# Optimization experiments

Measured on AMD Instinct MI355X. Metric: run time of the kernel, lower is better.

Reference implementation:

```python
import jax, jax.numpy as jnp
import numpy as np

NUM_CLASS = 3
SCORE_THRESH = 0.1
NMS_THRESH = 0.25
PRE = 512    # NMS_PRE_MAXSIZE (reduced from 4096 for memory; same algorithm)
POST = 100   # NMS_POST_MAXSIZE
EPS = 1e-8


def _cross(a, b):
    return a[..., 0] * b[..., 1] - a[..., 1] * b[..., 0]


def _corners(box):
    # box: (7,) = (x, y, z, dx, dy, dz, heading) -> BEV corners (4,2), CCW
    x, y, dx, dy, r = box[0], box[1], box[3], box[4], box[6]
    c, s = jnp.cos(r), jnp.sin(r)
    lx = jnp.array([0.5, -0.5, -0.5, 0.5]) * dx
    ly = jnp.array([0.5, 0.5, -0.5, -0.5]) * dy
    return jnp.stack([x + lx * c - ly * s, y + lx * s + ly * c], axis=-1)


def _in_box(pts, box):
    # pts (P,2): point-in-rotated-rect test in the box frame
    px, py = pts[:, 0] - box[0], pts[:, 1] - box[1]
    c, s = jnp.cos(box[6]), jnp.sin(box[6])
    u = px * c + py * s
    v = -px * s + py * c
    return (jnp.abs(u) <= box[3] * 0.5 + 1e-5) & (jnp.abs(v) <= box[4] * 0.5 + 1e-5)


def _bev_inter_area(ba, bb):
    # Exact rotated-rect intersection area (same construction as the CUDA
    # iou3d kernel: inside corners + edge intersections, angle-sorted shoelace).
    ca, cb = _corners(ba), _corners(bb)
    pa, ra = ca, jnp.roll(ca, -1, 0) - ca       # edges of a
    pb, rb = cb, jnp.roll(cb, -1, 0) - cb       # edges of b
    d = _cross(ra[:, None, :], rb[None, :, :])  # (4,4)
    dsafe = jnp.where(jnp.abs(d) > EPS, d, 1.0)
    qp = pb[None, :, :] - pa[:, None, :]
    t = _cross(qp, rb[None, :, :]) / dsafe
    u = _cross(qp, ra[:, None, :]) / dsafe
    vi = (jnp.abs(d) > EPS) & (t >= 0.0) & (t <= 1.0) & (u >= 0.0) & (u <= 1.0)
    ip = pa[:, None, :] + t[..., None] * ra[:, None, :]  # (4,4,2)
    pts = jnp.concatenate([ca, cb, ip.reshape(16, 2)], 0)          # (24,2)
    val = jnp.concatenate([_in_box(ca, bb), _in_box(cb, ba), vi.reshape(16)], 0)
    cnt = val.sum()
    ctr = (pts * val[:, None]).sum(0) / jnp.maximum(cnt, 1)
    ang = jnp.where(val, jnp.arctan2(pts[:, 1] - ctr[1], pts[:, 0] - ctr[0]), 1e9)
    o = jnp.argsort(ang)
    ps, vs = pts[o], val[o]
    ps = jnp.where(vs[:, None], ps, ps[0])  # collapse invalid onto first valid pt
    area = 0.5 * jnp.abs(_cross(ps, jnp.roll(ps, -1, 0)).sum())
    return jnp.where(cnt >= 3, area, 0.0)


def _iou3d(ba, bb):
    inter = _bev_inter_area(ba, bb)
    zt = jnp.minimum(ba[2] + ba[5] * 0.5, bb[2] + bb[5] * 0.5)
    zb = jnp.maximum(ba[2] - ba[5] * 0.5, bb[2] - bb[5] * 0.5)
    i3 = inter * jnp.maximum(zt - zb, 0.0)
    va = ba[3] * ba[4] * ba[5]
    vb = bb[3] * bb[4] * bb[5]
    return i3 / jnp.maximum(va + vb - i3, EPS)


_iou_mat = jax.vmap(jax.vmap(_iou3d, (None, 0)), (0, None))


def _nms(scores, boxes):
    # scores (K,) sorted descending; greedy suppression in score order
    valid = scores >= SCORE_THRESH
    iou = _iou_mat(boxes, boxes)  # (K,K)

    def body(sup, inp):
        row, v, i = inp
        keep = v & jnp.logical_not(sup[i])
        sup = sup | (keep & (row > NMS_THRESH))
        return sup, keep

    K = scores.shape[0]
    _, keep = jax.lax.scan(body, jnp.zeros((K,), bool), (iou, valid, jnp.arange(K)))
    return keep


def _post_one(cls_logits, boxes):
    # multi_classes_nms path: cls_preds_normalized=False -> sigmoid
    scores = jax.nn.sigmoid(cls_logits)  # (N, NUM_CLASS)
    out_b, out_s, out_l = [], [], []
    for k in range(NUM_CLASS):
        s = jnp.where(scores[:, k] >= SCORE_THRESH, scores[:, k], -1.0)
        top_s, idx = jax.lax.top_k(s, PRE)
        b = boxes[idx]
        keep = _nms(top_s, b)
        ks = jnp.where(keep, top_s, -1.0)
        os_, oi = jax.lax.top_k(ks, POST)
        ov = os_ >= SCORE_THRESH
        out_b.append(jnp.where(ov[:, None], b[oi], 0.0))
        out_s.append(jnp.where(ov, os_, 0.0))
        out_l.append((k + 1) * ov.astype(jnp.int32))  # final_labels = k + 1
    return (jnp.concatenate(out_b, 0), jnp.concatenate(out_s, 0),
            jnp.concatenate(out_l, 0))


def setup_inputs() -> dict:
    key = jax.random.key(0)
    k1, k2 = jax.random.split(key)
    B, N = 2, 100000
    batch_cls_preds = jax.random.normal(k1, (B, N, NUM_CLASS), dtype=jnp.float32)
    u = jax.random.uniform(k2, (B, N, 7), dtype=jnp.float32)
    x = u[..., 0] * 70.0
    y = u[..., 1] * 80.0 - 40.0
    z = u[..., 2] * 2.0 - 1.0
    dx = u[..., 3] * 3.0 + 1.5
    dy = u[..., 4] * 1.5 + 1.2
    dz = u[..., 5] * 1.0 + 1.3
    r = u[..., 6] * 2.0 * np.pi - np.pi
    batch_box_preds = jnp.stack([x, y, z, dx, dy, dz, r], axis=-1)
    return {"batch_cls_preds": batch_cls_preds, "batch_box_preds": batch_box_preds}


def reference(batch_cls_preds, batch_box_preds):
    # returns per-batch padded (pred_boxes (B, 3*POST, 7), pred_scores, pred_labels);
    # invalid slots are zeroed (label 0 == no detection)
    return jax.vmap(_post_one)(batch_cls_preds, batch_box_preds)
```

## Files before the change

kernel.cpp:

```cpp
#include <hip/hip_runtime.h>
#include <cstdint>

#define NCLS 3
#define NPTS 100000
#define NB 2
#define PRE 512
#define POST 100
#define SCORE_TH 0.1f
#define NMS_TH 0.25
#define CAP 1024
#define NBINS 384
#define XBIN_SH 16
#define XBIN_OFF (0xBFC00000u >> XBIN_SH)
#define XMARG 2e-3f
#define NPROB (NB * NCLS)
#define CPB 4
#define NKB 25
#define HPB (NCLS * NBINS)
#define BUFREG 1024
#define BUFSZ (NKB * BUFREG)
#define NCELL 36


__device__ __forceinline__ uint32_t score_key(float x)
{
    double sd = 1.0 / (1.0 + exp(-(double)x));
    float s = (float)sd;
    if (!(s >= SCORE_TH)) s = -1.0f;
    uint32_t u = __float_as_uint(s);
    return (u & 0x80000000u) ? ~u : (u | 0x80000000u);
}

__device__ __forceinline__ int xbin(float x)
{
    uint32_t u = __float_as_uint(x);
    uint32_t key = (u & 0x80000000u) ? ~u : (u | 0x80000000u);
    int b = (int)(key >> XBIN_SH) - (int)XBIN_OFF;
    return b < 0 ? 0 : (b > NBINS - 1 ? NBINS - 1 : b);
}

__global__ __launch_bounds__(1024) void hist_stage_kernel(
    const float* __restrict__ cls, uint32_t* __restrict__ hist_part,
    uint32_t* __restrict__ blkcnt, unsigned long long* __restrict__ buf)
{
    __shared__ uint32_t lh[NCLS][NBINS];
    __shared__ uint32_t lcnt3[NCLS];
    const int tid = threadIdx.x;
    for (int t = tid; t < NCLS * NBINS; t += 1024) ((uint32_t*)lh)[t] = 0;
    if (tid < NCLS) lcnt3[tid] = 0;
    __syncthreads();

    const int b = blockIdx.x / NKB, kb = blockIdx.x % NKB;
    const float* base = cls + (size_t)b * NPTS * NCLS;
    #pragma unroll
    for (int c = 0; c < CPB; ++c) {
        int i = (kb * CPB + c) * 1024 + tid;
        if (i < NPTS) {
            const float* cp = base + (size_t)i * NCLS;
            #pragma unroll
            for (int k = 0; k < NCLS; ++k) {
                float x = cp[k];
                int bn = xbin(x);
                if (bn > 0) atomicAdd(&lh[k][bn], 1u);
                if (xbin(x + XMARG) >= 1) {
                    uint32_t slot = atomicAdd(&lcnt3[k], 1u);
                    if (slot < BUFREG)
                        buf[(size_t)(b * NCLS + k) * BUFSZ + kb * BUFREG + slot]
                            = ((unsigned long long)__float_as_uint(x) << 32)
                            | (uint32_t)i;
                }
            }
        }
    }
    __syncthreads();
    uint32_t* P = hist_part + (size_t)blockIdx.x * HPB;
    for (int t = tid; t < HPB; t += 1024)
        P[t] = lh[t / NBINS][t % NBINS];
    if (tid < NCLS) {
        uint32_t c = lcnt3[tid];
        blkcnt[(b * NKB + kb) * NCLS + tid] = c < BUFREG ? c : BUFREG;
    }
}

__global__ __launch_bounds__(1024) void cell_kernel(
    const float* __restrict__ boxes, const uint32_t* __restrict__ hist_part,
    const uint32_t* __restrict__ blkcnt,
    const unsigned long long* __restrict__ buf,
    uint32_t* __restrict__ cand_idx, float* __restrict__ cand_score,
    unsigned long long* __restrict__ mask)
{
    const int blk = blockIdx.x;
    const int p = blk / NCELL;
    const int b = p / NCLS, k = p % NCLS;
    int cc = blk % NCELL;
    int wi = 0;
    while (cc >= 8 - wi) { cc -= 8 - wi; ++wi; }
    const int wj = wi + cc;
    const int tid = threadIdx.x;
    const int lane = tid & 63;
    const int wv = tid >> 6;

    __shared__ unsigned long long skey[CAP];
    __shared__ uint32_t sbins[NBINS];
    __shared__ double geo[128][20];
    __shared__ float scx[128], scy[128];
    __shared__ float sczlo[128], sczhi[128], scrad[128];
    __shared__ uint32_t lcnt, pivot_s;

    if (tid < NBINS) {
        uint32_t s = 0;
        const uint32_t* base2 = hist_part + (size_t)(b * NKB) * HPB
                              + k * NBINS + tid;
        #pragma unroll 5
        for (int kb = 0; kb < NKB; ++kb)
            s += base2[(size_t)kb * HPB];
        sbins[tid] = s;
    }
    if (tid == 0) { lcnt = 0; pivot_s = 0; }
    __syncthreads();
    for (int off = 1; off < NBINS; off <<= 1) {
        uint32_t v = 0;
        if (tid < NBINS && tid + off < NBINS) v = sbins[tid + off];
        __syncthreads();
        if (tid < NBINS) sbins[tid] += v;
        __syncthreads();
    }
    if (tid < NBINS && sbins[tid] >= PRE &&
        (tid == NBINS - 1 || sbins[tid + 1] < PRE))
        pivot_s = (uint32_t)tid;
    __syncthreads();
    int pb = (int)pivot_s;
    if (pb < 1) pb = 1;

    for (int r = 0; r < NKB; ++r) {
        const uint32_t c_r = blkcnt[(b * NKB + r) * NCLS + k];
        const unsigned long long* R = buf + (size_t)p * BUFSZ + r * BUFREG;
        for (uint32_t t = tid; t < c_r; t += 1024) {
            unsigned long long e = R[t];
            float x = __uint_as_float((uint32_t)(e >> 32));
            uint32_t i = (uint32_t)e;
            if (xbin(x + XMARG) >= pb) {
                uint32_t kk = score_key(x);
                uint32_t slot = atomicAdd(&lcnt, 1u);
                if (slot < CAP)
                    skey[slot] = ((unsigned long long)kk << 32)
                               | (uint32_t)(~i);
            }
        }
    }
    __syncthreads();
    const uint32_t cnt = lcnt < CAP ? lcnt : CAP;
    if (tid >= (int)cnt) skey[tid] = 0ull;
    __syncthreads();
    unsigned long long val = skey[tid];

    for (int k2 = 2; k2 <= CAP; k2 <<= 1) {
        const bool up = (tid & k2) == 0;
        for (int j = k2 >> 1; j >= 64; j >>= 1) {
            skey[tid] = val;
            __syncthreads();
            unsigned long long o = skey[tid ^ j];
            __syncthreads();
            const bool keepLarge = (((tid & j) == 0) == up);
            val = keepLarge ? (val >= o ? val : o) : (val <= o ? val : o);
        }
        int js = (k2 >> 1) < 32 ? (k2 >> 1) : 32;
        for (int j = js; j >= 1; j >>= 1) {
            unsigned long long o = __shfl_xor(val, j);
            const bool keepLarge = (((tid & j) == 0) == up);
            val = keepLarge ? (val >= o ? val : o) : (val <= o ? val : o);
        }
    }
    skey[tid] = val;
    __syncthreads();

    if (wi == 0 && wj == 0 && tid < PRE) {
        unsigned long long key = skey[tid];
        if (key == 0ull) {
            cand_idx[p * PRE + tid] = 0;
            cand_score[p * PRE + tid] = -1.0f;
        } else {
            uint32_t idx = ~((uint32_t)key);
            uint32_t ov = (uint32_t)(key >> 32);
            uint32_t ub = (ov & 0x80000000u) ? (ov ^ 0x80000000u) : ~ov;
            cand_idx[p * PRE + tid] = idx;
            cand_score[p * PRE + tid] = __uint_as_float(ub);
        }
    }

    if (tid < 128) {
        const int row = (tid < 64) ? (wi * 64 + tid) : (wj * 64 + (tid - 64));
        unsigned long long key = skey[row];
        double* D = geo[tid];
        if (key == 0ull) {
            #pragma unroll
            for (int m = 0; m < 20; ++m) D[m] = 0.0;
            scx[tid] = 0.0f; scy[tid] = 0.0f;
            sczlo[tid] = 0.0f; sczhi[tid] = 0.0f; scrad[tid] = 0.0f;
        } else {
            uint32_t idx = ~((uint32_t)key);
            const float* bp = boxes + ((size_t)b * NPTS + idx) * 7;
            double x = bp[0], y = bp[1], z = bp[2];
            double dx = bp[3], dy = bp[4], dz = bp[5], r = bp[6];
            double c = cos(r), s = sin(r);
            double hx = 0.5 * dx, hy = 0.5 * dy;
            double zlo = z - 0.5 * dz, zhi = z + 0.5 * dz;
            double rad = sqrt(hx * hx + hy * hy);
            D[0] = x; D[1] = y; D[2] = c; D[3] = s; D[4] = hx; D[5] = hy;
            D[6] = zlo; D[7] = zhi; D[8] = dx * dy * dz; D[9] = rad;
            const double lxs[4] = { hx, -hx, -hx,  hx };
            const double lys[4] = { hy,  hy, -hy, -hy };
            #pragma unroll
            for (int m = 0; m < 4; ++m) {
                D[10 + m] = x + lxs[m] * c - lys[m] * s;
                D[14 + m] = y + lxs[m] * s + lys[m] * c;
            }
            scx[tid] = (float)x; scy[tid] = (float)y;
            sczlo[tid] = (float)zlo; sczhi[tid] = (float)zhi;
            scrad[tid] = (float)rad;
        }
    }
    __syncthreads();

    for (int rr = wv; rr < 64; rr += 16) {
        const int bi = wi * 64 + rr;
        const int j = wj * 64 + lane;

        bool surv = false;
        if (j > bi) {
            float hz = fminf(sczhi[rr], sczhi[64 + lane])
                     - fmaxf(sczlo[rr], sczlo[64 + lane]);
            if (hz > 0.0f) {
                float ddx = scx[rr] - scx[64 + lane];
                float ddy = scy[rr] - scy[64 + lane];
                float rs = scrad[rr] + scrad[64 + lane] + 0.01f;
                surv = (ddx * ddx + ddy * ddy <= rs * rs);
            }
        }
        unsigned long long sm = __ballot(surv);
        unsigned long long supw = 0ull;
        const double* A = geo[rr];

        while (sm) {
            int jb = __ffsll(sm) - 1;
            sm &= sm - 1ull;
            const double* B = geo[64 + jb];

            double hzd = fmin(A[7], B[7]) - fmax(A[6], B[6]);
            if (hzd <= 0.0) continue;
            {
                double ddx = B[0] - A[0], ddy = B[1] - A[1];
                double ca = A[2], sa = A[3], cb2 = B[2], sb2 = B[3];
                double cd = fabs(ca * cb2 + sa * sb2);
                double sd = fabs(sa * cb2 - ca * sb2);
                double pax = fabs(ddx * ca + ddy * sa);
                double pay = fabs(-ddx * sa + ddy * ca);
                double pbx = fabs(ddx * cb2 + ddy * sb2);
                double pby = fabs(-ddx * sb2 + ddy * cb2);
                if (pax > A[4] + B[4] * cd + B[5] * sd) continue;
                if (pay > A[5] + B[4] * sd + B[5] * cd) continue;
                if (pbx > B[4] + A[4] * cd + A[5] * sd) continue;
                if (pby > B[5] + A[4] * sd + A[5] * cd) continue;
                double areaA = 4.0 * A[4] * A[5], areaB = 4.0 * B[4] * B[5];
                double i3m = fmin(areaA, areaB) * hzd;
                double den = A[8] + B[8] - i3m;
                if (den < 1e-8) den = 1e-8;
                if (!(i3m / den > (double)NMS_TH)) continue;
            }

            double PX = 0.0, PY = 0.0;
            bool valid = false;
            if (lane < 8) {
                const double* S = (lane < 4) ? A : B;
                const double* O = (lane < 4) ? B : A;
                int m = lane & 3;
                PX = S[10 + m]; PY = S[14 + m];
                double rx = PX - O[0], ry = PY - O[1];
                double u =  rx * O[2] + ry * O[3];
                double v = -rx * O[3] + ry * O[2];
                valid = (fabs(u) <= O[4] + 1e-5) && (fabs(v) <= O[5] + 1e-5);
            } else if (lane < 24) {
                int e = lane - 8, m = e >> 2, nn = e & 3;
                double ax = A[10 + m], ay = A[14 + m];
                double rax = A[10 + ((m + 1) & 3)] - ax;
                double ray = A[14 + ((m + 1) & 3)] - ay;
                double bx = B[10 + nn], by = B[14 + nn];
                double rbx = B[10 + ((nn + 1) & 3)] - bx;
                double rby = B[14 + ((nn + 1) & 3)] - by;
                double d = rax * rby - ray * rbx;
                if (fabs(d) > 1e-8) {
                    double qx = bx - ax, qy = by - ay;
                    double tt = (qx * rby - qy * rbx) / d;
                    double uu = (qx * ray - qy * rax) / d;
                    valid = (tt >= 0.0 && tt <= 1.0 && uu >= 0.0 && uu <= 1.0);
                    PX = ax + tt * rax; PY = ay + tt * ray;
                }
            }
            if (!valid) { PX = 0.0; PY = 0.0; }

            unsigned long long bal = __ballot(valid);
            int cntv = __popcll(bal);
            double sx = PX, sy = PY;
            #pragma unroll
            for (int off = 16; off; off >>= 1) {
                sx += __shfl_xor(sx, off);
                sy += __shfl_xor(sy, off);
            }
            int cdiv = cntv > 0 ? cntv : 1;
            double cxc = sx / cdiv, cyc = sy / cdiv;

            double ang = valid ? atan2(PY - cyc, PX - cxc) : 1e9;
            int sidx = lane;

            #pragma unroll
            for (int kk2 = 2; kk2 <= 32; kk2 <<= 1) {
                #pragma unroll
                for (int jj = kk2 >> 1; jj > 0; jj >>= 1) {
                    double oang = __shfl_xor(ang, jj);
                    double opx  = __shfl_xor(PX, jj);
                    double opy  = __shfl_xor(PY, jj);
                    int    oidx = __shfl_xor(sidx, jj);
                    bool iLow = (lane & jj) == 0;
                    bool dirUp = (lane & kk2) == 0;
                    bool mineFirst = (ang < oang) || (ang == oang && sidx < oidx);
                    bool keepMine = (mineFirst == (iLow == dirUp));
                    if (!keepMine) { ang = oang; PX = opx; PY = opy; sidx = oidx; }
                }
            }

            double nxp = __shfl(PX, (lane + 1) & 31);
            double nyp = __shfl(PY, (lane + 1) & 31);
            double fx  = __shfl(PX, 0);
            double fy  = __shfl(PY, 0);
            bool last = (lane == cntv - 1);
            double qx = last ? fx : nxp, qy = last ? fy : nyp;
            double contrib = 0.0;
            if (lane < cntv)
                contrib = (PX - cxc) * (qy - cyc) - (PY - cyc) * (qx - cxc);
            #pragma unroll
            for (int off = 16; off; off >>= 1)
                contrib += __shfl_xor(contrib, off);
            double inter = (cntv >= 3) ? 0.5 * fabs(contrib) : 0.0;

            if (lane == 0) {
                double zt = fmin(A[7], B[7]);
                double zb = fmax(A[6], B[6]);
                double hz = zt - zb;
                bool sup = false;
                if (hz > 0.0) {
                    double i3 = inter * hz;
                    double den = A[8] + B[8] - i3;
                    if (den < 1e-8) den = 1e-8;
                    sup = (i3 / den) > (double)NMS_TH;
                }
                if (sup) supw |= 1ull << jb;
            }
        }

        if (lane == 0)
            mask[(size_t)(p * PRE + bi) * 8 + wj] = supw;
    }
}

__global__ __launch_bounds__(256) void nms_out_kernel(
    const float* __restrict__ boxes, const uint32_t* __restrict__ cand_idx,
    const float* __restrict__ cand_score,
    const unsigned long long* __restrict__ mask, float* __restrict__ out)
{
    const int p = blockIdx.x;
    const int b = p / NCLS, k = p % NCLS;
    const int tid = threadIdx.x;

    __shared__ unsigned long long smask[PRE * 8];
    __shared__ float sscore[PRE];
    __shared__ int slist[POST];
    __shared__ int scnt;

    for (int w = tid; w < PRE * 8; w += 256)
        smask[w] = mask[(size_t)p * PRE * 8 + w];
    for (int i = tid; i < PRE; i += 256)
        sscore[i] = cand_score[p * PRE + i];
    __syncthreads();

    if (tid < 64) {
        const int ln = tid;
        unsigned long long rem = 0ull;
        #pragma unroll
        for (int w = 0; w < 8; ++w) {
            unsigned long long bw = __ballot(sscore[w * 64 + ln] >= SCORE_TH);
            if (ln == w) rem = bw;
        }
        int c = 0;
        for (;;) {
            int cv = rem ? ((ln << 6) + (__ffsll(rem) - 1)) : 4096;
            int o1 = __shfl_xor(cv, 1); cv = cv < o1 ? cv : o1;
            int o2 = __shfl_xor(cv, 2); cv = cv < o2 ? cv : o2;
            int o4 = __shfl_xor(cv, 4); cv = cv < o4 ? cv : o4;
            int i = __shfl(cv, 0);
            if (i >= 4096) break;
            if (ln == 0) slist[c] = i;
            ++c;
            if (c >= POST) break;
            unsigned long long mm = (ln < 8) ? smask[i * 8 + ln] : 0ull;
            if (ln == (i >> 6)) mm |= 1ull << (i & 63);
            rem &= ~mm;
        }
        if (ln == 0) scnt = c;
    }
    __syncthreads();

    const int cnt2 = scnt;
    for (int t2 = tid; t2 < POST; t2 += 256) {
        int row = b * (NCLS * POST) + k * POST + t2;
        float* ob = out + (size_t)row * 7;
        float* os = out + (size_t)NB * NCLS * POST * 7 + row;
        float* ol = out + (size_t)NB * NCLS * POST * 7 + (size_t)NB * NCLS * POST + row;
        if (t2 < cnt2) {
            int rr = slist[t2];
            uint32_t idx = cand_idx[p * PRE + rr];
            const float* bp = boxes + ((size_t)b * NPTS + idx) * 7;
            #pragma unroll
            for (int c7 = 0; c7 < 7; ++c7) ob[c7] = bp[c7];
            *os = sscore[rr];
            *ol = (float)(k + 1);
        } else {
            #pragma unroll
            for (int c7 = 0; c7 < 7; ++c7) ob[c7] = 0.0f;
            *os = 0.0f;
            *ol = 0.0f;
        }
    }
}

extern "C" void kernel_launch(void* const* d_in, const int* in_sizes, int n_in,
                              void* d_out, int out_size, void* d_ws, size_t ws_size,
                              hipStream_t stream)
{
    (void)in_sizes; (void)n_in; (void)out_size; (void)ws_size;
    const float* cls   = (const float*)d_in[0];
    const float* boxes = (const float*)d_in[1];
    float* out = (float*)d_out;

    char* ws = (char*)d_ws;
    uint32_t* hist_part   = (uint32_t*)(ws);
    uint32_t* blkcnt      = (uint32_t*)(ws + 230400);
    unsigned long long* buf = (unsigned long long*)(ws + 231424);
    uint32_t* cand_idx    = (uint32_t*)(ws + 1460224);
    float*    cand_score  = (float*)   (ws + 1472512);
    unsigned long long* mask = (unsigned long long*)(ws + 1484800);

    hipLaunchKernelGGL(hist_stage_kernel, dim3(NB * NKB), dim3(1024), 0,
                       stream, cls, hist_part, blkcnt, buf);
    hipLaunchKernelGGL(cell_kernel, dim3(NPROB * NCELL), dim3(1024), 0,
                       stream, boxes, hist_part, blkcnt, buf,
                       cand_idx, cand_score, mask);
    hipLaunchKernelGGL(nms_out_kernel, dim3(NPROB), dim3(256), 0, stream,
                       boxes, cand_idx, cand_score, mask, out);
}
```

Before: 139.7 us.

## Replace bitonic sort with rank counting and wave-level scan for pivot

Swaps the 1024-element shared-memory bitonic sort for a rank-by-counting pass, where each candidate counts how many keys exceed it and scatters itself straight to its output slot and geometry tile. The block-wide Hillis-Steele prefix scan over histogram bins is replaced by a single-wave shuffle scan with ballot to find the pivot bin. Block counts are cached in shared memory and the candidate buffer read becomes one guarded load per region. The aim is to cut the many barriers of the sort and scan. The price is O(cnt) shared-memory reads per thread, which costs more when the candidate count is large.

```diff
diff --git a/kernel.cpp b/kernel.cpp
--- a/kernel.cpp
+++ b/kernel.cpp
@@ -102,11 +102,23 @@
 
     __shared__ unsigned long long skey[CAP];
     __shared__ uint32_t sbins[NBINS];
+    __shared__ uint32_t sblk[NKB];
     __shared__ double geo[128][20];
     __shared__ float scx[128], scy[128];
     __shared__ float sczlo[128], sczhi[128], scrad[128];
-    __shared__ uint32_t lcnt, pivot_s;
-
+    __shared__ uint32_t lcnt;
+
+    for (int t = tid; t < 128 * 20; t += 1024) ((double*)geo)[t] = 0.0;
+    if (tid < 128) {
+        scx[tid] = 0.0f; scy[tid] = 0.0f;
+        sczlo[tid] = 0.0f; sczhi[tid] = 0.0f; scrad[tid] = 0.0f;
+    }
+    if (wi == 0 && wj == 0 && tid < PRE) {
+        cand_idx[p * PRE + tid] = 0;
+        cand_score[p * PRE + tid] = -1.0f;
+    }
+    if (tid < NKB) sblk[tid] = blkcnt[(b * NKB + tid) * NCLS + k];
+    if (tid == 0) lcnt = 0;
     if (tid < NBINS) {
         uint32_t s = 0;
         const uint32_t* base2 = hist_part + (size_t)(b * NKB) * HPB
@@ -116,27 +128,32 @@
             s += base2[(size_t)kb * HPB];
         sbins[tid] = s;
     }
-    if (tid == 0) { lcnt = 0; pivot_s = 0; }
-    __syncthreads();
-    for (int off = 1; off < NBINS; off <<= 1) {
-        uint32_t v = 0;
-        if (tid < NBINS && tid + off < NBINS) v = sbins[tid + off];
-        __syncthreads();
-        if (tid < NBINS) sbins[tid] += v;
-        __syncthreads();
-    }
-    if (tid < NBINS && sbins[tid] >= PRE &&
-        (tid == NBINS - 1 || sbins[tid + 1] < PRE))
-        pivot_s = (uint32_t)tid;
-    __syncthreads();
-    int pb = (int)pivot_s;
-    if (pb < 1) pb = 1;
+    __syncthreads();
+
+    int pb;
+    {
+        int pbw = -1;
+        uint32_t carry = 0;
+        #pragma unroll
+        for (int c = 5; c >= 0; --c) {
+            uint32_t v = sbins[c * 64 + lane];
+            #pragma unroll
+            for (int off = 1; off < 64; off <<= 1) {
+                uint32_t o = __shfl_down(v, off);
+                v += (lane + off < 64) ? o : 0u;
+            }
+            uint32_t full = v + carry;
+            unsigned long long bal = __ballot(full >= PRE);
+            if (pbw < 0 && bal)
+                pbw = c * 64 + (63 - __clzll((long long)bal));
+            carry += (uint32_t)__shfl((int)v, 0);
+        }
+        pb = pbw < 1 ? 1 : pbw;
+    }
 
     for (int r = 0; r < NKB; ++r) {
-        const uint32_t c_r = blkcnt[(b * NKB + r) * NCLS + k];
-        const unsigned long long* R = buf + (size_t)p * BUFSZ + r * BUFREG;
-        for (uint32_t t = tid; t < c_r; t += 1024) {
-            unsigned long long e = R[t];
+        if (tid < (int)sblk[r]) {
+            unsigned long long e = buf[(size_t)p * BUFSZ + r * BUFREG + tid];
             float x = __uint_as_float((uint32_t)(e >> 32));
             uint32_t i = (uint32_t)e;
             if (xbin(x + XMARG) >= pb) {
@@ -149,56 +166,27 @@
         }
     }
     __syncthreads();
-    const uint32_t cnt = lcnt < CAP ? lcnt : CAP;
-    if (tid >= (int)cnt) skey[tid] = 0ull;
-    __syncthreads();
-    unsigned long long val = skey[tid];
-
-    for (int k2 = 2; k2 <= CAP; k2 <<= 1) {
-        const bool up = (tid & k2) == 0;
-        for (int j = k2 >> 1; j >= 64; j >>= 1) {
-            skey[tid] = val;
-            __syncthreads();
-            unsigned long long o = skey[tid ^ j];
-            __syncthreads();
-            const bool keepLarge = (((tid & j) == 0) == up);
-            val = keepLarge ? (val >= o ? val : o) : (val <= o ? val : o);
-        }
-        int js = (k2 >> 1) < 32 ? (k2 >> 1) : 32;
-        for (int j = js; j >= 1; j >>= 1) {
-            unsigned long long o = __shfl_xor(val, j);
-            const bool keepLarge = (((tid & j) == 0) == up);
-            val = keepLarge ? (val >= o ? val : o) : (val <= o ? val : o);
-        }
-    }
-    skey[tid] = val;
-    __syncthreads();
-
-    if (wi == 0 && wj == 0 && tid < PRE) {
-        unsigned long long key = skey[tid];
-        if (key == 0ull) {
-            cand_idx[p * PRE + tid] = 0;
-            cand_score[p * PRE + tid] = -1.0f;
-        } else {
-            uint32_t idx = ~((uint32_t)key);
-            uint32_t ov = (uint32_t)(key >> 32);
+    const int cnt = (int)(lcnt < CAP ? lcnt : CAP);
+
+    unsigned long long mykey = (tid < cnt) ? skey[tid] : 0ull;
+    int rank = 0;
+    if (tid < cnt)
+        for (int j = 0; j < cnt; ++j)
+            rank += (skey[j] > mykey) ? 1 : 0;
+
+    if (tid < cnt) {
+        uint32_t idx = ~((uint32_t)mykey);
+        if (wi == 0 && wj == 0 && rank < PRE) {
+            uint32_t ov = (uint32_t)(mykey >> 32);
             uint32_t ub = (ov & 0x80000000u) ? (ov ^ 0x80000000u) : ~ov;
-            cand_idx[p * PRE + tid] = idx;
-            cand_score[p * PRE + tid] = __uint_as_float(ub);
-        }
-    }
-
-    if (tid < 128) {
-        const int row = (tid < 64) ? (wi * 64 + tid) : (wj * 64 + (tid - 64));
-        unsigned long long key = skey[row];
-        double* D = geo[tid];
-        if (key == 0ull) {
-            #pragma unroll
-            for (int m = 0; m < 20; ++m) D[m] = 0.0;
-            scx[tid] = 0.0f; scy[tid] = 0.0f;
-            sczlo[tid] = 0.0f; sczhi[tid] = 0.0f; scrad[tid] = 0.0f;
-        } else {
-            uint32_t idx = ~((uint32_t)key);
+            cand_idx[p * PRE + rank] = idx;
+            cand_score[p * PRE + rank] = __uint_as_float(ub);
+        }
+        const int slotA = rank - wi * 64;
+        const int slotB = rank - wj * 64;
+        const bool inA = (slotA >= 0 && slotA < 64);
+        const bool inB = (slotB >= 0 && slotB < 64);
+        if (inA || inB) {
             const float* bp = boxes + ((size_t)b * NPTS + idx) * 7;
             double x = bp[0], y = bp[1], z = bp[2];
             double dx = bp[3], dy = bp[4], dz = bp[5], r = bp[6];
@@ -206,18 +194,30 @@
             double hx = 0.5 * dx, hy = 0.5 * dy;
             double zlo = z - 0.5 * dz, zhi = z + 0.5 * dz;
             double rad = sqrt(hx * hx + hy * hy);
-            D[0] = x; D[1] = y; D[2] = c; D[3] = s; D[4] = hx; D[5] = hy;
-            D[6] = zlo; D[7] = zhi; D[8] = dx * dy * dz; D[9] = rad;
+            double V[20];
+            V[0] = x; V[1] = y; V[2] = c; V[3] = s; V[4] = hx; V[5] = hy;
+            V[6] = zlo; V[7] = zhi; V[8] = dx * dy * dz; V[9] = rad;
             const double lxs[4] = { hx, -hx, -hx,  hx };
             const double lys[4] = { hy,  hy, -hy, -hy };
             #pragma unroll
             for (int m = 0; m < 4; ++m) {
-                D[10 + m] = x + lxs[m] * c - lys[m] * s;
-                D[14 + m] = y + lxs[m] * s + lys[m] * c;
-            }
-            scx[tid] = (float)x; scy[tid] = (float)y;
-            sczlo[tid] = (float)zlo; sczhi[tid] = (float)zhi;
-            scrad[tid] = (float)rad;
+                V[10 + m] = x + lxs[m] * c - lys[m] * s;
+                V[14 + m] = y + lxs[m] * s + lys[m] * c;
+            }
+            if (inA) {
+                #pragma unroll
+                for (int m = 0; m < 20; ++m) geo[slotA][m] = V[m];
+                scx[slotA] = (float)x; scy[slotA] = (float)y;
+                sczlo[slotA] = (float)zlo; sczhi[slotA] = (float)zhi;
+                scrad[slotA] = (float)rad;
+            }
+            if (inB) {
+                #pragma unroll
+                for (int m = 0; m < 20; ++m) geo[64 + slotB][m] = V[m];
+                scx[64 + slotB] = (float)x; scy[64 + slotB] = (float)y;
+                sczlo[64 + slotB] = (float)zlo; sczhi[64 + slotB] = (float)zhi;
+                scrad[64 + slotB] = (float)rad;
+            }
         }
     }
     __syncthreads();
```

New measurement: 141.9 us. Within noise of the previous version (+1.6%).
